# Optimization experiments

Measured on AMD Instinct MI355X. Metric: run time of the kernel, lower is better.

## Reference

```python
import jax, jax.numpy as jnp
import numpy as np
from jax import lax

BETA = 0.95     # snn.Leaky(0.95)
THRESH = 1.0    # snntorch default threshold
ALPHA = 2.0     # snntorch ATan surrogate default alpha
NUM_STEPS = 100

@jax.custom_vjp
def spike_fn(u):
    return (u > 0).astype(u.dtype)

def _spike_fwd(u):
    return (u > 0).astype(u.dtype), u

def _spike_bwd(u, g):
    surr = (ALPHA / 2.0) / (1.0 + (jnp.pi / 2.0 * ALPHA * u) ** 2)
    return (g * surr,)

spike_fn.defvjp(_spike_fwd, _spike_bwd)

def leaky_scan(inputs, mem0):
    # inputs: [T, ...]; snntorch Leaky with reset_mechanism='zero'
    def step(carry, x_t):
        mem, _ = carry
        reset = spike_fn(mem - THRESH)       # spike detected from previous mem
        base = BETA * mem + x_t
        mem = base - reset * base            # zero-reset
        spk = spike_fn(mem - THRESH)
        return (mem, spk), None
    (mem, spk), _ = lax.scan(step, (mem0, jnp.zeros_like(mem0)), inputs)
    return spk, mem

def setup_inputs():
    key = jax.random.key(0)
    ks = jax.random.split(key, 7)
    B, T, W, C = 32, 2000, 512, 4
    H, O = 1024, 10
    s = lambda n: 1.0 / np.sqrt(n)
    return {
        "x": jax.random.normal(ks[0], (B, T, W, C), jnp.float32),
        "conv_w": jax.random.uniform(ks[1], (C,), jnp.float32, -s(C), s(C)),
        "conv_b": jax.random.uniform(ks[2], (), jnp.float32, -s(C), s(C)),
        "hidden_w": jax.random.uniform(ks[3], (H, W), jnp.float32, -s(W), s(W)),
        "hidden_b": jax.random.uniform(ks[4], (H,), jnp.float32, -s(W), s(W)),
        "out_w": jax.random.uniform(ks[5], (O, H), jnp.float32, -s(H), s(H)),
        "out_b": jax.random.uniform(ks[6], (O,), jnp.float32, -s(H), s(H)),
    }

def reference(x, conv_w, conv_b, hidden_w, hidden_b, out_w, out_b):
    B, T, W, _ = x.shape
    # 1x1 conv fusing 4 antenna channels: (B,T,W,4)->(B,T,W)
    fused = jnp.einsum('bhwc,c->bhw', x, conv_w) + conv_b
    G = T // NUM_STEPS
    fused = fused.reshape(B, G, NUM_STEPS, W)      # [B,G,S,W]
    seq1 = jnp.moveaxis(fused, 2, 0)               # [S,B,G,W] time-major
    spk, _ = leaky_scan(seq1, jnp.zeros((B, G, W), x.dtype))
    hidden = spk @ hidden_w.T + hidden_b           # [B,G,H]
    seq2 = jnp.moveaxis(hidden, 1, 0)              # [G,B,H]
    spk2, _ = leaky_scan(seq2, jnp.zeros((B, hidden.shape[2]), x.dtype))
    out = spk2 @ out_w.T + out_b                   # [B,O]
    return jax.nn.softmax(out, axis=1)
```

## Files before the change

kernel.cpp:

```cpp
#include <hip/hip_runtime.h>
#include <hip/hip_bf16.h>

typedef float f32x4 __attribute__((ext_vector_type(4)));

#define NB 32
#define NT 2000
#define NW 512
#define NG 20
#define NS 100
#define NH 1024
#define NO 10
#define BETA 0.95f
#define THRESH 1.0f

__global__ __launch_bounds__(256) void k1_conv_scan(
    const f32x4* __restrict__ x,
    const float* __restrict__ cw,
    const float* __restrict__ cb,
    float* __restrict__ spk1)
{
    int bid = blockIdx.x;
    int half = bid & 1;
    int bg = bid >> 1;
    int g = bg % NG;
    int b = bg / NG;
    int tid = threadIdx.x;

    const f32x4* __restrict__ base =
        x + ((size_t)(b * NT + g * NS) * NW + half * 256);

    float w0 = cw[0], w1 = cw[1], w2 = cw[2], w3 = cw[3];
    float bias = cb[0];

    f32x4 A[10], B[10];
    float mem = 0.0f;

#define LOAD10(dst, S0)                                                        \
    {                                                                          \
        _Pragma("unroll")                                                      \
        for (int j = 0; j < 10; ++j)                                           \
            dst[j] = __builtin_nontemporal_load(base + (tid + ((S0) + j) * NW)); \
    }
#define STEP10(src)                                                            \
    {                                                                          \
        _Pragma("unroll")                                                      \
        for (int j = 0; j < 10; ++j) {                                         \
            f32x4 v = src[j];                                                  \
            float f = fmaf(v[0], w0, fmaf(v[1], w1,                            \
                      fmaf(v[2], w2, fmaf(v[3], w3, bias))));                  \
            float base_m = fmaf(BETA, mem, f);                                 \
            mem = (mem > THRESH) ? 0.0f : base_m;                              \
        }                                                                      \
    }

    LOAD10(A, 0)
    LOAD10(B, 10) STEP10(A)
    LOAD10(A, 20) STEP10(B)
    LOAD10(B, 30) STEP10(A)
    LOAD10(A, 40) STEP10(B)
    LOAD10(B, 50) STEP10(A)
    LOAD10(A, 60) STEP10(B)
    LOAD10(B, 70) STEP10(A)
    LOAD10(A, 80) STEP10(B)
    LOAD10(B, 90) STEP10(A)
    STEP10(B)
#undef LOAD10
#undef STEP10

    spk1[(b * NG + g) * NW + half * 256 + tid] = (mem > THRESH) ? 1.0f : 0.0f;
}

__global__ __launch_bounds__(256) void k_transpose(
    const float* __restrict__ wsrc,
    float* __restrict__ wT)
{
    __shared__ float tile[32][33];
    int bk = blockIdx.x;
    int bh = blockIdx.y;
    int tx = threadIdx.x;
    int ty = threadIdx.y;
    #pragma unroll
    for (int j = 0; j < 4; ++j)
        tile[ty + j * 8][tx] = wsrc[(bh * 32 + ty + j * 8) * NW + bk * 32 + tx];
    __syncthreads();
    #pragma unroll
    for (int j = 0; j < 4; ++j)
        wT[(bk * 32 + ty + j * 8) * NH + bh * 32 + tx] = tile[tx][ty + j * 8];
}

__global__ __launch_bounds__(256) void k2_hidden_scan(
    const float* __restrict__ spk1,
    const float* __restrict__ wT,
    const float* __restrict__ hb,
    float* __restrict__ spk2)
{
    __shared__ float sk[NG][NW];
    __shared__ float red[4][NG][64];

    int bid = blockIdx.x;
    int b = bid >> 4;
    int hgrp = bid & 15;
    int t = threadIdx.x;
    int lane = t & 63;
    int c = t >> 6;
    int h = hgrp * 64 + lane;

    {
        const f32x4* __restrict__ sp4 =
            (const f32x4*)(spk1 + (size_t)b * NG * NW);
        f32x4* sk4 = (f32x4*)&sk[0][0];
        #pragma unroll
        for (int i = 0; i < 10; ++i)
            sk4[t + i * 256] = sp4[t + i * 256];
    }
    __syncthreads();

    float acc[NG];
    #pragma unroll
    for (int g = 0; g < NG; ++g) acc[g] = 0.0f;

    int k0 = c * 128;
    #pragma unroll 4
    for (int kk = k0; kk < k0 + 128; kk += 4) {
        float a0 = wT[(kk + 0) * NH + h];
        float a1 = wT[(kk + 1) * NH + h];
        float a2 = wT[(kk + 2) * NH + h];
        float a3 = wT[(kk + 3) * NH + h];
        #pragma unroll
        for (int g = 0; g < NG; ++g) {
            f32x4 u = *(const f32x4*)&sk[g][kk];
            acc[g] = fmaf(u[0], a0, fmaf(u[1], a1,
                     fmaf(u[2], a2, fmaf(u[3], a3, acc[g]))));
        }
    }

    #pragma unroll
    for (int g = 0; g < NG; ++g) red[c][g][lane] = acc[g];
    __syncthreads();

    if (t < 64) {
        float hbias = hb[h];
        float mem = 0.0f;
        #pragma unroll
        for (int g = 0; g < NG; ++g) {
            float xin = red[0][g][lane] + red[1][g][lane]
                      + red[2][g][lane] + red[3][g][lane] + hbias;
            float base = fmaf(BETA, mem, xin);
            mem = (mem > THRESH) ? 0.0f : base;
        }
        spk2[b * NH + h] = (mem > THRESH) ? 1.0f : 0.0f;
    }
}

__global__ __launch_bounds__(256) void k3_out(
    const float* __restrict__ spk2,
    const float* __restrict__ ow,
    const float* __restrict__ ob,
    float* __restrict__ out)
{
    int b = blockIdx.x;
    int t = threadIdx.x;

    float p[NO];
    #pragma unroll
    for (int o = 0; o < NO; ++o) p[o] = 0.0f;

    for (int h = t; h < NH; h += 256) {
        float s = spk2[b * NH + h];
        #pragma unroll
        for (int o = 0; o < NO; ++o) p[o] += s * ow[o * NH + h];
    }

    __shared__ float red[NO][256];
    #pragma unroll
    for (int o = 0; o < NO; ++o) red[o][t] = p[o];
    __syncthreads();

    for (int off = 128; off > 0; off >>= 1) {
        if (t < off) {
            #pragma unroll
            for (int o = 0; o < NO; ++o) red[o][t] += red[o][t + off];
        }
        __syncthreads();
    }

    if (t == 0) {
        float v[NO], mx = -1e30f;
        #pragma unroll
        for (int o = 0; o < NO; ++o) { v[o] = red[o][0] + ob[o]; mx = fmaxf(mx, v[o]); }
        float sum = 0.0f;
        #pragma unroll
        for (int o = 0; o < NO; ++o) { v[o] = expf(v[o] - mx); sum += v[o]; }
        float inv = 1.0f / sum;
        #pragma unroll
        for (int o = 0; o < NO; ++o) out[b * NO + o] = v[o] * inv;
    }
}

extern "C" void kernel_launch(void* const* d_in, const int* in_sizes, int n_in,
                              void* d_out, int out_size, void* d_ws, size_t ws_size,
                              hipStream_t stream) {
    const f32x4*  x  = (const f32x4*)d_in[0];
    const float*  cw = (const float*)d_in[1];
    const float*  cb = (const float*)d_in[2];
    const float*  hw = (const float*)d_in[3];
    const float*  hb = (const float*)d_in[4];
    const float*  ow = (const float*)d_in[5];
    const float*  ob = (const float*)d_in[6];
    float* out = (float*)d_out;

    char* ws = (char*)d_ws;
    float* spk1 = (float*)(ws);
    float* wT   = (float*)(ws + 1310720);
    float* spk2 = (float*)(ws + 1310720 + 2097152);

    k_transpose<<<dim3(16, 32), dim3(32, 8), 0, stream>>>(hw, wT);

    k1_conv_scan<<<(NB * NG * NW) / 256, 256, 0, stream>>>(x, cw, cb, spk1);

    k2_hidden_scan<<<NB * 16, 256, 0, stream>>>(spk1, wT, hb, spk2);

    k3_out<<<NB, 256, 0, stream>>>(spk2, ow, ob, out);
}
```

Before: 120.2 us.

## Fuse weight transpose into conv-scan kernel and widen hidden GEMV tiles

The standalone weight transpose kernel is merged into the conv/scan kernel as 512 extra blocks, removing one launch and letting the transpose overlap with the bandwidth-bound scan. The hidden-layer kernel now computes 4 hidden units per thread with vectorized f32x4 weight loads, uses 8 K-slices of 64, and halves the grid to 256 blocks. Partial sums are reduced in two shared-memory passes to fit the smaller buffer. The trade is fewer blocks (lower occupancy) and more accumulator registers in exchange for better weight-load efficiency.

```diff
diff --git a/kernel.cpp b/kernel.cpp
--- a/kernel.cpp
+++ b/kernel.cpp
@@ -13,27 +13,32 @@
 #define BETA 0.95f
 #define THRESH 1.0f
 
-__global__ __launch_bounds__(256) void k1_conv_scan(
+__global__ __launch_bounds__(256) void k1_conv_scan_tr(
     const f32x4* __restrict__ x,
     const float* __restrict__ cw,
     const float* __restrict__ cb,
-    float* __restrict__ spk1)
+    float* __restrict__ spk1,
+    const float* __restrict__ wsrc,
+    float* __restrict__ wT)
 {
+    __shared__ float tile[32][33];
     int bid = blockIdx.x;
-    int half = bid & 1;
-    int bg = bid >> 1;
-    int g = bg % NG;
-    int b = bg / NG;
-    int tid = threadIdx.x;
-
-    const f32x4* __restrict__ base =
-        x + ((size_t)(b * NT + g * NS) * NW + half * 256);
-
-    float w0 = cw[0], w1 = cw[1], w2 = cw[2], w3 = cw[3];
-    float bias = cb[0];
-
-    f32x4 A[10], B[10];
-    float mem = 0.0f;
+
+    if (bid < 1280) {
+        int half = bid & 1;
+        int bg = bid >> 1;
+        int g = bg % NG;
+        int b = bg / NG;
+        int tid = threadIdx.x;
+
+        const f32x4* __restrict__ base =
+            x + ((size_t)(b * NT + g * NS) * NW + half * 256);
+
+        float w0 = cw[0], w1 = cw[1], w2 = cw[2], w3 = cw[3];
+        float bias = cb[0];
+
+        f32x4 A[10], B[10];
+        float mem = 0.0f;
 
 #define LOAD10(dst, S0)                                                        \
     {                                                                          \
@@ -53,39 +58,35 @@
         }                                                                      \
     }
 
-    LOAD10(A, 0)
-    LOAD10(B, 10) STEP10(A)
-    LOAD10(A, 20) STEP10(B)
-    LOAD10(B, 30) STEP10(A)
-    LOAD10(A, 40) STEP10(B)
-    LOAD10(B, 50) STEP10(A)
-    LOAD10(A, 60) STEP10(B)
-    LOAD10(B, 70) STEP10(A)
-    LOAD10(A, 80) STEP10(B)
-    LOAD10(B, 90) STEP10(A)
-    STEP10(B)
+        LOAD10(A, 0)
+        LOAD10(B, 10) STEP10(A)
+        LOAD10(A, 20) STEP10(B)
+        LOAD10(B, 30) STEP10(A)
+        LOAD10(A, 40) STEP10(B)
+        LOAD10(B, 50) STEP10(A)
+        LOAD10(A, 60) STEP10(B)
+        LOAD10(B, 70) STEP10(A)
+        LOAD10(A, 80) STEP10(B)
+        LOAD10(B, 90) STEP10(A)
+        STEP10(B)
 #undef LOAD10
 #undef STEP10
 
-    spk1[(b * NG + g) * NW + half * 256 + tid] = (mem > THRESH) ? 1.0f : 0.0f;
-}
-
-__global__ __launch_bounds__(256) void k_transpose(
-    const float* __restrict__ wsrc,
-    float* __restrict__ wT)
-{
-    __shared__ float tile[32][33];
-    int bk = blockIdx.x;
-    int bh = blockIdx.y;
-    int tx = threadIdx.x;
-    int ty = threadIdx.y;
-    #pragma unroll
-    for (int j = 0; j < 4; ++j)
-        tile[ty + j * 8][tx] = wsrc[(bh * 32 + ty + j * 8) * NW + bk * 32 + tx];
-    __syncthreads();
-    #pragma unroll
-    for (int j = 0; j < 4; ++j)
-        wT[(bk * 32 + ty + j * 8) * NH + bh * 32 + tx] = tile[tx][ty + j * 8];
+        spk1[(b * NG + g) * NW + half * 256 + tid] = (mem > THRESH) ? 1.0f : 0.0f;
+    } else {
+        int tbid = bid - 1280;
+        int bk = tbid & 15;
+        int bh = tbid >> 4;
+        int tx = threadIdx.x & 31;
+        int ty = threadIdx.x >> 5;
+        #pragma unroll
+        for (int j = 0; j < 4; ++j)
+            tile[ty + j * 8][tx] = wsrc[(bh * 32 + ty + j * 8) * NW + bk * 32 + tx];
+        __syncthreads();
+        #pragma unroll
+        for (int j = 0; j < 4; ++j)
+            wT[(bk * 32 + ty + j * 8) * NH + bh * 32 + tx] = tile[tx][ty + j * 8];
+    }
 }
 
 __global__ __launch_bounds__(256) void k2_hidden_scan(
@@ -95,15 +96,15 @@
     float* __restrict__ spk2)
 {
     __shared__ float sk[NG][NW];
-    __shared__ float red[4][NG][64];
+    __shared__ f32x4 red[4][10][32];
 
     int bid = blockIdx.x;
-    int b = bid >> 4;
-    int hgrp = bid & 15;
+    int b = bid >> 3;
+    int hgrp = bid & 7;
     int t = threadIdx.x;
-    int lane = t & 63;
-    int c = t >> 6;
-    int h = hgrp * 64 + lane;
+    int lane5 = t & 31;
+    int c = t >> 5;
+    int h = hgrp * 128 + lane5 * 4;
 
     {
         const f32x4* __restrict__ sp4 =
@@ -115,41 +116,67 @@
     }
     __syncthreads();
 
-    float acc[NG];
-    #pragma unroll
-    for (int g = 0; g < NG; ++g) acc[g] = 0.0f;
-
-    int k0 = c * 128;
-    #pragma unroll 4
-    for (int kk = k0; kk < k0 + 128; kk += 4) {
-        float a0 = wT[(kk + 0) * NH + h];
-        float a1 = wT[(kk + 1) * NH + h];
-        float a2 = wT[(kk + 2) * NH + h];
-        float a3 = wT[(kk + 3) * NH + h];
+    f32x4 acc[NG];
+    #pragma unroll
+    for (int g = 0; g < NG; ++g)
+        #pragma unroll
+        for (int j = 0; j < 4; ++j) acc[g][j] = 0.0f;
+
+    int k0 = c * 64;
+    #pragma unroll 2
+    for (int kkg = 0; kkg < 16; ++kkg) {
+        int kk = k0 + kkg * 4;
+        f32x4 w0 = *(const f32x4*)&wT[(kk + 0) * NH + h];
+        f32x4 w1 = *(const f32x4*)&wT[(kk + 1) * NH + h];
+        f32x4 w2 = *(const f32x4*)&wT[(kk + 2) * NH + h];
+        f32x4 w3 = *(const f32x4*)&wT[(kk + 3) * NH + h];
         #pragma unroll
         for (int g = 0; g < NG; ++g) {
             f32x4 u = *(const f32x4*)&sk[g][kk];
-            acc[g] = fmaf(u[0], a0, fmaf(u[1], a1,
-                     fmaf(u[2], a2, fmaf(u[3], a3, acc[g]))));
-        }
-    }
-
-    #pragma unroll
-    for (int g = 0; g < NG; ++g) red[c][g][lane] = acc[g];
-    __syncthreads();
-
-    if (t < 64) {
-        float hbias = hb[h];
-        float mem = 0.0f;
-        #pragma unroll
-        for (int g = 0; g < NG; ++g) {
-            float xin = red[0][g][lane] + red[1][g][lane]
-                      + red[2][g][lane] + red[3][g][lane] + hbias;
-            float base = fmaf(BETA, mem, xin);
-            mem = (mem > THRESH) ? 0.0f : base;
-        }
-        spk2[b * NH + h] = (mem > THRESH) ? 1.0f : 0.0f;
-    }
+            #pragma unroll
+            for (int j = 0; j < 4; ++j)
+                acc[g][j] = fmaf(u[0], w0[j], fmaf(u[1], w1[j],
+                            fmaf(u[2], w2[j], fmaf(u[3], w3[j], acc[g][j]))));
+        }
+    }
+
+    float hbias = 0.0f, mem = 0.0f;
+    if (t < 128) hbias = hb[hgrp * 128 + t];
+    int hl4 = t >> 2, hj = t & 3;
+
+    #pragma unroll
+    for (int half = 0; half < 2; ++half) {
+        __syncthreads();
+        if (c < 4) {
+            #pragma unroll
+            for (int gg = 0; gg < 10; ++gg)
+                red[c][gg][lane5] = acc[half * 10 + gg];
+        }
+        __syncthreads();
+        if (c >= 4) {
+            #pragma unroll
+            for (int gg = 0; gg < 10; ++gg) {
+                f32x4 v = red[c - 4][gg][lane5];
+                f32x4 a = acc[half * 10 + gg];
+                #pragma unroll
+                for (int j = 0; j < 4; ++j) v[j] += a[j];
+                red[c - 4][gg][lane5] = v;
+            }
+        }
+        __syncthreads();
+        if (t < 128) {
+            #pragma unroll
+            for (int gg = 0; gg < 10; ++gg) {
+                float xin = red[0][gg][hl4][hj] + red[1][gg][hl4][hj]
+                          + red[2][gg][hl4][hj] + red[3][gg][hl4][hj] + hbias;
+                float base = fmaf(BETA, mem, xin);
+                mem = (mem > THRESH) ? 0.0f : base;
+            }
+        }
+    }
+
+    if (t < 128)
+        spk2[b * NH + hgrp * 128 + t] = (mem > THRESH) ? 1.0f : 0.0f;
 }
 
 __global__ __launch_bounds__(256) void k3_out(
@@ -214,11 +241,9 @@
     float* wT   = (float*)(ws + 1310720);
     float* spk2 = (float*)(ws + 1310720 + 2097152);
 
-    k_transpose<<<dim3(16, 32), dim3(32, 8), 0, stream>>>(hw, wT);
-
-    k1_conv_scan<<<(NB * NG * NW) / 256, 256, 0, stream>>>(x, cw, cb, spk1);
-
-    k2_hidden_scan<<<NB * 16, 256, 0, stream>>>(spk1, wT, hb, spk2);
+    k1_conv_scan_tr<<<1792, 256, 0, stream>>>(x, cw, cb, spk1, hw, wT);
+
+    k2_hidden_scan<<<NB * 8, 256, 0, stream>>>(spk1, wT, hb, spk2);
 
     k3_out<<<NB, 256, 0, stream>>>(spk2, ow, ob, out);
 }
```

Measured after the change: 110.8 us. -7.8%, faster.
